# Kernel optimization log

Hardware: AMD Instinct MI355X
Metric: run time of the kernel (lower is better)

## Reference

```python
import jax, jax.numpy as jnp
import numpy as np

DIM = 1024
B, S = 4, 4096

def setup_inputs() -> dict:
    key = jax.random.key(0)
    ks = jax.random.split(key, 8)
    scale = 1.0 / np.sqrt(DIM)
    x = jax.random.normal(ks[0], (B, S, DIM), dtype=jnp.float32)
    Wk = jax.random.normal(ks[1], (DIM, DIM), dtype=jnp.float32) * scale
    Wv = jax.random.normal(ks[2], (DIM, DIM), dtype=jnp.float32) * scale
    Wr = jax.random.normal(ks[3], (DIM, DIM), dtype=jnp.float32) * scale
    Wo = jax.random.normal(ks[4], (DIM, DIM), dtype=jnp.float32) * scale
    time_decay = jax.random.normal(ks[5], (DIM,), dtype=jnp.float32) * 0.01 - 5.0
    time_first = jax.random.normal(ks[6], (DIM,), dtype=jnp.float32) * 0.01
    return {"x": x, "Wk": Wk, "Wv": Wv, "Wr": Wr, "Wo": Wo,
            "time_decay": time_decay, "time_first": time_first}

def reference(x, Wk, Wv, Wr, Wo, time_decay, time_first):
    # Projections (Linear with weight [out, in]: y = x @ W^T)
    k = jnp.einsum('bsd,ed->bse', x, Wk)
    v = jnp.einsum('bsd,ed->bse', x, Wv)
    r = jax.nn.sigmoid(jnp.einsum('bsd,ed->bse', x, Wr))
    w = -jnp.exp(time_decay)          # (D,)
    decay = jnp.exp(w)                # exp(w), per-channel decay in (0,1)
    eu = jnp.exp(time_first)          # exp(u)
    kv = k * v                        # (B, S, D)

    def step(state, kv_t):
        wkv = state + eu * kv_t       # output numerator this step
        new_state = decay * state + kv_t
        return new_state, wkv

    state0 = jnp.zeros((x.shape[0], x.shape[2]), dtype=x.dtype)
    # scan over time axis: move S to leading dim
    _, wkv_seq = jax.lax.scan(step, state0, jnp.swapaxes(kv, 0, 1))  # (S, B, D)
    out = r * jnp.swapaxes(wkv_seq, 0, 1)  # (B, S, D)
    return jnp.einsum('bsd,ed->bse', out, Wo)
```

## Files before the change

### kernel.cpp

```cpp
#include <hip/hip_runtime.h>
#include <hip/hip_bf16.h>

#define DIMD   1024
#define BATCH  4
#define SEQ    4096
#define NTOK   (BATCH * SEQ)
#define CHUNK  64
#define NCHUNK (SEQ / CHUNK)

#define BM 128
#define BN 128
#define BK 32
#define BNF 64

typedef unsigned short ushort_t;
typedef __attribute__((ext_vector_type(8))) __bf16   bf16x8;
typedef __attribute__((ext_vector_type(4))) float    f32x4;
typedef __attribute__((ext_vector_type(8))) ushort_t u16x8;

__device__ __forceinline__ float b2f(ushort_t u) {
    union { unsigned int i; float f; } x;
    x.i = ((unsigned int)u) << 16;
    return x.f;
}

__device__ __forceinline__ ushort_t f2b(float f) {
    union { float f; unsigned int i; } x;
    x.f = f;
    unsigned int r = x.i + 0x7fffu + ((x.i >> 16) & 1u);
    return (ushort_t)(r >> 16);
}

__global__ __launch_bounds__(256)
void conv_f2b(const float* __restrict__ src, ushort_t* __restrict__ dst, int n8)
{
    const int i = blockIdx.x * 256 + threadIdx.x;
    if (i >= n8) return;
    const float4* s4 = (const float4*)src;
    const float4 a = s4[i * 2];
    const float4 b = s4[i * 2 + 1];
    u16x8 o;
    o[0] = f2b(a.x); o[1] = f2b(a.y); o[2] = f2b(a.z); o[3] = f2b(a.w);
    o[4] = f2b(b.x); o[5] = f2b(b.y); o[6] = f2b(b.z); o[7] = f2b(b.w);
    *(u16x8*)(dst + (size_t)i * 8) = o;
}

__global__ __launch_bounds__(256)
void conv_w(const float* __restrict__ W0, const float* __restrict__ W1,
            const float* __restrict__ W2, const float* __restrict__ W3,
            ushort_t* __restrict__ dst)
{
    const int m = blockIdx.y;
    const float* src = (m == 0) ? W0 : (m == 1) ? W1 : (m == 2) ? W2 : W3;
    const int i = blockIdx.x * 256 + threadIdx.x;
    const float4* s4 = (const float4*)src;
    const float4 a = s4[i * 2];
    const float4 b = s4[i * 2 + 1];
    u16x8 o;
    o[0] = f2b(a.x); o[1] = f2b(a.y); o[2] = f2b(a.z); o[3] = f2b(a.w);
    o[4] = f2b(b.x); o[5] = f2b(b.y); o[6] = f2b(b.z); o[7] = f2b(b.w);
    *(u16x8*)(dst + (size_t)m * DIMD * DIMD + (size_t)i * 8) = o;
}

__global__ __launch_bounds__(256, 2)
void gemm_kvr(const ushort_t* __restrict__ A,
              const ushort_t* __restrict__ Wk,
              const ushort_t* __restrict__ Wv,
              const ushort_t* __restrict__ Wr,
              const float* __restrict__ td,
              ushort_t* __restrict__ Okv,
              ushort_t* __restrict__ Or,
              float* __restrict__ cs)
{
    __shared__ __align__(16) ushort_t As[BM * BK];
    __shared__ __align__(16) ushort_t Bk[BNF * BK];
    __shared__ __align__(16) ushort_t Bv[BNF * BK];
    __shared__ __align__(16) ushort_t Br[BNF * BK];

    const int tid  = threadIdx.x;
    const int lane = tid & 63;
    const int wv   = tid >> 6;
    const int wr   = wv >> 1;
    const int wc   = wv & 1;
    const int lrow = lane & 15;
    const int kq   = lane >> 4;

    const int row0 = blockIdx.x * BM;
    const int e0   = blockIdx.y * BNF;

    f32x4 ak[4][2], av[4][2], ar[4][2];
#pragma unroll
    for (int i = 0; i < 4; i++)
#pragma unroll
        for (int j = 0; j < 2; j++) {
            ak[i][j] = f32x4{0.f, 0.f, 0.f, 0.f};
            av[i][j] = f32x4{0.f, 0.f, 0.f, 0.f};
            ar[i][j] = f32x4{0.f, 0.f, 0.f, 0.f};
        }

    for (int kt = 0; kt < DIMD / BK; ++kt) {
        const int k0 = kt * BK;

        __syncthreads();

#pragma unroll
        for (int it = 0; it < 2; ++it) {
            const int chunk = tid + it * 256;
            const int r = chunk >> 2;
            const int c = (chunk & 3) << 3;
            const ushort_t* ga = A + (size_t)(row0 + r) * DIMD + k0 + c;
            __builtin_amdgcn_global_load_lds(
                (__attribute__((address_space(1))) void*)ga,
                (__attribute__((address_space(3))) void*)((char*)As + chunk * 16),
                16, 0, 0);
        }
        {
            const int r = tid >> 2;
            const int c = (tid & 3) << 3;
            const size_t go = (size_t)(e0 + r) * DIMD + k0 + c;
            __builtin_amdgcn_global_load_lds(
                (__attribute__((address_space(1))) void*)(Wk + go),
                (__attribute__((address_space(3))) void*)((char*)Bk + tid * 16),
                16, 0, 0);
            __builtin_amdgcn_global_load_lds(
                (__attribute__((address_space(1))) void*)(Wv + go),
                (__attribute__((address_space(3))) void*)((char*)Bv + tid * 16),
                16, 0, 0);
            __builtin_amdgcn_global_load_lds(
                (__attribute__((address_space(1))) void*)(Wr + go),
                (__attribute__((address_space(3))) void*)((char*)Br + tid * 16),
                16, 0, 0);
        }

        __syncthreads();

        bf16x8 af[4], bk4[2], bv4[2], br4[2];
#pragma unroll
        for (int i = 0; i < 4; i++)
            af[i] = *(const bf16x8*)(As + (wr * 64 + i * 16 + lrow) * BK + kq * 8);
#pragma unroll
        for (int j = 0; j < 2; j++) {
            const int bo = (wc * 32 + j * 16 + lrow) * BK + kq * 8;
            bk4[j] = *(const bf16x8*)(Bk + bo);
            bv4[j] = *(const bf16x8*)(Bv + bo);
            br4[j] = *(const bf16x8*)(Br + bo);
        }

#pragma unroll
        for (int i = 0; i < 4; i++)
#pragma unroll
            for (int j = 0; j < 2; j++) {
                ak[i][j] = __builtin_amdgcn_mfma_f32_16x16x32_bf16(
                    af[i], bk4[j], ak[i][j], 0, 0, 0);
                av[i][j] = __builtin_amdgcn_mfma_f32_16x16x32_bf16(
                    af[i], bv4[j], av[i][j], 0, 0, 0);
                ar[i][j] = __builtin_amdgcn_mfma_f32_16x16x32_bf16(
                    af[i], br4[j], ar[i][j], 0, 0, 0);
            }
    }

#pragma unroll
    for (int i = 0; i < 4; i++)
#pragma unroll
        for (int j = 0; j < 2; j++)
#pragma unroll
            for (int r = 0; r < 4; r++) {
                const int row = row0 + wr * 64 + i * 16 + kq * 4 + r;
                const int col = e0 + wc * 32 + j * 16 + lrow;
                const size_t o = (size_t)row * DIMD + col;
                Okv[o] = f2b(ak[i][j][r] * av[i][j][r]);
                Or[o]  = f2b(1.f / (1.f + __expf(-ar[i][j][r])));
            }

#pragma unroll
    for (int j = 0; j < 2; j++) {
        const int col = e0 + wc * 32 + j * 16 + lrow;
        const float w = -__expf(td[col]);
        float s = 0.f;
#pragma unroll
        for (int i = 0; i < 4; i++)
#pragma unroll
            for (int r = 0; r < 4; r++) {
                const int rl = i * 16 + kq * 4 + r;
                s += __expf(w * (float)(63 - rl)) * ak[i][j][r] * av[i][j][r];
            }
        s += __shfl_xor(s, 16);
        s += __shfl_xor(s, 32);
        if (kq == 0) {
            const int gchunk = (row0 >> 6) + wr;
            cs[(size_t)gchunk * DIMD + col] = s;
        }
    }
}

__global__ __launch_bounds__(256, 2)
void gemm_bt(const ushort_t* __restrict__ A,
             const ushort_t* __restrict__ W,
             float* __restrict__ Of)
{
    __shared__ __align__(16) ushort_t As[BM * BK];
    __shared__ __align__(16) ushort_t Bs[BN * BK];

    const int tid  = threadIdx.x;
    const int lane = tid & 63;
    const int wv   = tid >> 6;
    const int wr   = wv >> 1;
    const int wc   = wv & 1;
    const int lrow = lane & 15;
    const int kq   = lane >> 4;

    const int row0 = blockIdx.x * BM;
    const int e0   = blockIdx.y * BN;

    f32x4 acc[4][4];
#pragma unroll
    for (int i = 0; i < 4; i++)
#pragma unroll
        for (int j = 0; j < 4; j++)
            acc[i][j] = f32x4{0.f, 0.f, 0.f, 0.f};

    for (int kt = 0; kt < DIMD / BK; ++kt) {
        const int k0 = kt * BK;

        __syncthreads();

#pragma unroll
        for (int it = 0; it < 2; ++it) {
            const int chunk = tid + it * 256;
            const int r = chunk >> 2;
            const int c = (chunk & 3) << 3;
            const ushort_t* ga = A + (size_t)(row0 + r) * DIMD + k0 + c;
            const ushort_t* gb = W + (size_t)(e0 + r) * DIMD + k0 + c;
            __builtin_amdgcn_global_load_lds(
                (__attribute__((address_space(1))) void*)ga,
                (__attribute__((address_space(3))) void*)((char*)As + chunk * 16),
                16, 0, 0);
            __builtin_amdgcn_global_load_lds(
                (__attribute__((address_space(1))) void*)gb,
                (__attribute__((address_space(3))) void*)((char*)Bs + chunk * 16),
                16, 0, 0);
        }

        __syncthreads();

        bf16x8 af[4], bfr[4];
#pragma unroll
        for (int i = 0; i < 4; i++)
            af[i] = *(const bf16x8*)(As + (wr * 64 + i * 16 + lrow) * BK + kq * 8);
#pragma unroll
        for (int j = 0; j < 4; j++)
            bfr[j] = *(const bf16x8*)(Bs + (wc * 64 + j * 16 + lrow) * BK + kq * 8);

#pragma unroll
        for (int i = 0; i < 4; i++)
#pragma unroll
            for (int j = 0; j < 4; j++)
                acc[i][j] = __builtin_amdgcn_mfma_f32_16x16x32_bf16(
                    af[i], bfr[j], acc[i][j], 0, 0, 0);
    }

#pragma unroll
    for (int i = 0; i < 4; i++)
#pragma unroll
        for (int j = 0; j < 4; j++)
#pragma unroll
            for (int r = 0; r < 4; r++) {
                const int row = row0 + wr * 64 + i * 16 + kq * 4 + r;
                const int col = e0 + wc * 64 + j * 16 + lrow;
                Of[(size_t)row * DIMD + col] = acc[i][j][r];
            }
}

__global__ __launch_bounds__(256)
void chunk_scan(float* __restrict__ cs, const float* __restrict__ td)
{
    const int idx = blockIdx.x * 256 + threadIdx.x;
    const int d = idx & (DIMD - 1);
    const int b = idx >> 10;

    const float w      = -__expf(td[d]);
    const float decayL = __expf(w * (float)CHUNK);

    float v[NCHUNK];
    const size_t base = ((size_t)b * NCHUNK) * DIMD + d;
#pragma unroll
    for (int c = 0; c < NCHUNK; c++)
        v[c] = cs[base + (size_t)c * DIMD];

    float st = 0.f;
#pragma unroll
    for (int c = 0; c < NCHUNK; c++) {
        const float sc = v[c];
        v[c] = st;
        st = decayL * st + sc;
    }

#pragma unroll
    for (int c = 0; c < NCHUNK; c++)
        cs[base + (size_t)c * DIMD] = v[c];
}

__global__ __launch_bounds__(256)
void emit(const ushort_t* __restrict__ kvb, const ushort_t* __restrict__ rb,
          const float* __restrict__ td, const float* __restrict__ tf,
          const float* __restrict__ cs, ushort_t* __restrict__ op)
{
    const int t  = blockIdx.x * 256 + threadIdx.x;
    const int d0 = (t & (DIMD / 8 - 1)) * 8;
    const int bc = t >> 7;
    const int c  = bc & (NCHUNK - 1);
    const int b  = bc >> 6;

    float decay[8], eu[8], st[8];
#pragma unroll
    for (int j = 0; j < 8; j++) {
        decay[j] = __expf(-__expf(td[d0 + j]));
        eu[j]    = __expf(tf[d0 + j]);
    }
    const float* csp = cs + ((size_t)bc * DIMD + d0);
    const float4 s0 = *(const float4*)csp;
    const float4 s1 = *(const float4*)(csp + 4);
    st[0] = s0.x; st[1] = s0.y; st[2] = s0.z; st[3] = s0.w;
    st[4] = s1.x; st[5] = s1.y; st[6] = s1.z; st[7] = s1.w;

    size_t off = ((size_t)b * SEQ + (size_t)c * CHUNK) * DIMD + d0;
#pragma unroll 8
    for (int i = 0; i < CHUNK; i++) {
        const u16x8 kv8 = *(const u16x8*)(kvb + off);
        const u16x8 r8  = *(const u16x8*)(rb + off);
        u16x8 o8;
#pragma unroll
        for (int j = 0; j < 8; j++) {
            const float kv = b2f(kv8[j]);
            o8[j] = f2b(b2f(r8[j]) * (st[j] + eu[j] * kv));
            st[j] = decay[j] * st[j] + kv;
        }
        *(u16x8*)(op + off) = o8;
        off += DIMD;
    }
}

extern "C" void kernel_launch(void* const* d_in, const int* in_sizes, int n_in,
                              void* d_out, int out_size, void* d_ws, size_t ws_size,
                              hipStream_t stream)
{
    const float* x  = (const float*)d_in[0];
    const float* Wk = (const float*)d_in[1];
    const float* Wv = (const float*)d_in[2];
    const float* Wr = (const float*)d_in[3];
    const float* Wo = (const float*)d_in[4];
    const float* td = (const float*)d_in[5];
    const float* tf = (const float*)d_in[6];

    ushort_t* xb  = (ushort_t*)d_ws;
    ushort_t* Wb  = xb + (size_t)NTOK * DIMD;
    ushort_t* Wkb = Wb;
    ushort_t* Wvb = Wb + (size_t)DIMD * DIMD;
    ushort_t* Wrb = Wb + 2 * (size_t)DIMD * DIMD;
    ushort_t* Wob = Wb + 3 * (size_t)DIMD * DIMD;
    float*    cs  = (float*)(Wb + 4 * (size_t)DIMD * DIMD);
    ushort_t* pbuf = xb;

    ushort_t* kvb = (ushort_t*)d_out;
    ushort_t* rb  = kvb + (size_t)NTOK * DIMD;
    float*    out = (float*)d_out;

    conv_f2b<<<NTOK * DIMD / 8 / 256, 256, 0, stream>>>(x, xb, NTOK * DIMD / 8);
    conv_w<<<dim3(DIMD * DIMD / 8 / 256, 4), 256, 0, stream>>>(Wk, Wv, Wr, Wo, Wb);

    gemm_kvr<<<dim3(NTOK / BM, DIMD / BNF), 256, 0, stream>>>(
        xb, Wkb, Wvb, Wrb, td, kvb, rb, cs);

    chunk_scan<<<BATCH * DIMD / 256, 256, 0, stream>>>(cs, td);

    emit<<<BATCH * NCHUNK * (DIMD / 8) / 256, 256, 0, stream>>>(
        kvb, rb, td, tf, cs, pbuf);

    gemm_bt<<<dim3(NTOK / BM, DIMD / BN), 256, 0, stream>>>(pbuf, Wob, out);
}
```

Before: 319.9 us.

## Merge conversion kernels, enlarge kvr GEMM tile, fold chunk scan into emit

Combines the x and weight bf16 conversion kernels into a single launch. Doubles the gemm_kvr row tile to 256 with 512-thread blocks (8 waves) so each staged weight tile is reused across more rows. Removes the separate chunk_scan kernel: each emit thread recomputes its starting state by sequentially folding the preceding chunk sums. This drops two launches and a read-write pass over cs, at the cost of redundant O(chunk index) work per emit thread and possible occupancy pressure from launch_bounds(512,4).

```diff
diff --git a/kernel.cpp b/kernel.cpp
--- a/kernel.cpp
+++ b/kernel.cpp
@@ -8,10 +8,11 @@
 #define CHUNK  64
 #define NCHUNK (SEQ / CHUNK)
 
+#define BMF 256
+#define BNF 64
 #define BM 128
 #define BN 128
 #define BK 32
-#define BNF 64
 
 typedef unsigned short ushort_t;
 typedef __attribute__((ext_vector_type(8))) __bf16   bf16x8;
@@ -31,38 +32,37 @@
     return (ushort_t)(r >> 16);
 }
 
+#define XU (NTOK * DIMD / 8)
+#define WU (DIMD * DIMD / 8)
 __global__ __launch_bounds__(256)
-void conv_f2b(const float* __restrict__ src, ushort_t* __restrict__ dst, int n8)
+void conv_all(const float* __restrict__ x,
+              const float* __restrict__ W0, const float* __restrict__ W1,
+              const float* __restrict__ W2, const float* __restrict__ W3,
+              ushort_t* __restrict__ xb, ushort_t* __restrict__ Wb)
 {
     const int i = blockIdx.x * 256 + threadIdx.x;
-    if (i >= n8) return;
+    const float* src;
+    ushort_t* dst;
+    int u;
+    if (i < XU) {
+        src = x; dst = xb; u = i;
+    } else {
+        const int wi = i - XU;
+        const int m = wi >> 17;
+        u = wi & (WU - 1);
+        src = (m == 0) ? W0 : (m == 1) ? W1 : (m == 2) ? W2 : W3;
+        dst = Wb + (size_t)m * DIMD * DIMD;
+    }
     const float4* s4 = (const float4*)src;
-    const float4 a = s4[i * 2];
-    const float4 b = s4[i * 2 + 1];
+    const float4 a = s4[(size_t)u * 2];
+    const float4 b = s4[(size_t)u * 2 + 1];
     u16x8 o;
     o[0] = f2b(a.x); o[1] = f2b(a.y); o[2] = f2b(a.z); o[3] = f2b(a.w);
     o[4] = f2b(b.x); o[5] = f2b(b.y); o[6] = f2b(b.z); o[7] = f2b(b.w);
-    *(u16x8*)(dst + (size_t)i * 8) = o;
-}
-
-__global__ __launch_bounds__(256)
-void conv_w(const float* __restrict__ W0, const float* __restrict__ W1,
-            const float* __restrict__ W2, const float* __restrict__ W3,
-            ushort_t* __restrict__ dst)
-{
-    const int m = blockIdx.y;
-    const float* src = (m == 0) ? W0 : (m == 1) ? W1 : (m == 2) ? W2 : W3;
-    const int i = blockIdx.x * 256 + threadIdx.x;
-    const float4* s4 = (const float4*)src;
-    const float4 a = s4[i * 2];
-    const float4 b = s4[i * 2 + 1];
-    u16x8 o;
-    o[0] = f2b(a.x); o[1] = f2b(a.y); o[2] = f2b(a.z); o[3] = f2b(a.w);
-    o[4] = f2b(b.x); o[5] = f2b(b.y); o[6] = f2b(b.z); o[7] = f2b(b.w);
-    *(u16x8*)(dst + (size_t)m * DIMD * DIMD + (size_t)i * 8) = o;
-}
-
-__global__ __launch_bounds__(256, 2)
+    *(u16x8*)(dst + (size_t)u * 8) = o;
+}
+
+__global__ __launch_bounds__(512, 4)
 void gemm_kvr(const ushort_t* __restrict__ A,
               const ushort_t* __restrict__ Wk,
               const ushort_t* __restrict__ Wv,
@@ -72,7 +72,7 @@
               ushort_t* __restrict__ Or,
               float* __restrict__ cs)
 {
-    __shared__ __align__(16) ushort_t As[BM * BK];
+    __shared__ __align__(16) ushort_t As[BMF * BK];
     __shared__ __align__(16) ushort_t Bk[BNF * BK];
     __shared__ __align__(16) ushort_t Bv[BNF * BK];
     __shared__ __align__(16) ushort_t Br[BNF * BK];
@@ -80,12 +80,12 @@
     const int tid  = threadIdx.x;
     const int lane = tid & 63;
     const int wv   = tid >> 6;
-    const int wr   = wv >> 1;
-    const int wc   = wv & 1;
+    const int wr   = wv & 3;
+    const int wc   = wv >> 2;
     const int lrow = lane & 15;
     const int kq   = lane >> 4;
 
-    const int row0 = blockIdx.x * BM;
+    const int row0 = blockIdx.x * BMF;
     const int e0   = blockIdx.y * BNF;
 
     f32x4 ak[4][2], av[4][2], ar[4][2];
@@ -105,7 +105,7 @@
 
 #pragma unroll
         for (int it = 0; it < 2; ++it) {
-            const int chunk = tid + it * 256;
+            const int chunk = tid + it * 512;
             const int r = chunk >> 2;
             const int c = (chunk & 3) << 3;
             const ushort_t* ga = A + (size_t)(row0 + r) * DIMD + k0 + c;
@@ -114,7 +114,7 @@
                 (__attribute__((address_space(3))) void*)((char*)As + chunk * 16),
                 16, 0, 0);
         }
-        {
+        if (tid < 256) {
             const int r = tid >> 2;
             const int c = (tid & 3) << 3;
             const size_t go = (size_t)(e0 + r) * DIMD + k0 + c;
@@ -123,12 +123,17 @@
                 (__attribute__((address_space(3))) void*)((char*)Bk + tid * 16),
                 16, 0, 0);
             __builtin_amdgcn_global_load_lds(
-                (__attribute__((address_space(1))) void*)(Wv + go),
-                (__attribute__((address_space(3))) void*)((char*)Bv + tid * 16),
-                16, 0, 0);
-            __builtin_amdgcn_global_load_lds(
                 (__attribute__((address_space(1))) void*)(Wr + go),
                 (__attribute__((address_space(3))) void*)((char*)Br + tid * 16),
+                16, 0, 0);
+        } else {
+            const int t2 = tid - 256;
+            const int r = t2 >> 2;
+            const int c = (t2 & 3) << 3;
+            const size_t go = (size_t)(e0 + r) * DIMD + k0 + c;
+            __builtin_amdgcn_global_load_lds(
+                (__attribute__((address_space(1))) void*)(Wv + go),
+                (__attribute__((address_space(3))) void*)((char*)Bv + t2 * 16),
                 16, 0, 0);
         }
 
@@ -187,7 +192,7 @@
         s += __shfl_xor(s, 16);
         s += __shfl_xor(s, 32);
         if (kq == 0) {
-            const int gchunk = (row0 >> 6) + wr;
+            const int gchunk = blockIdx.x * 4 + wr;
             cs[(size_t)gchunk * DIMD + col] = s;
         }
     }
@@ -272,35 +277,6 @@
 }
 
 __global__ __launch_bounds__(256)
-void chunk_scan(float* __restrict__ cs, const float* __restrict__ td)
-{
-    const int idx = blockIdx.x * 256 + threadIdx.x;
-    const int d = idx & (DIMD - 1);
-    const int b = idx >> 10;
-
-    const float w      = -__expf(td[d]);
-    const float decayL = __expf(w * (float)CHUNK);
-
-    float v[NCHUNK];
-    const size_t base = ((size_t)b * NCHUNK) * DIMD + d;
-#pragma unroll
-    for (int c = 0; c < NCHUNK; c++)
-        v[c] = cs[base + (size_t)c * DIMD];
-
-    float st = 0.f;
-#pragma unroll
-    for (int c = 0; c < NCHUNK; c++) {
-        const float sc = v[c];
-        v[c] = st;
-        st = decayL * st + sc;
-    }
-
-#pragma unroll
-    for (int c = 0; c < NCHUNK; c++)
-        cs[base + (size_t)c * DIMD] = v[c];
-}
-
-__global__ __launch_bounds__(256)
 void emit(const ushort_t* __restrict__ kvb, const ushort_t* __restrict__ rb,
           const float* __restrict__ td, const float* __restrict__ tf,
           const float* __restrict__ cs, ushort_t* __restrict__ op)
@@ -311,17 +287,25 @@
     const int c  = bc & (NCHUNK - 1);
     const int b  = bc >> 6;
 
-    float decay[8], eu[8], st[8];
+    float w[8], decay[8], decayL[8], eu[8], st[8];
 #pragma unroll
     for (int j = 0; j < 8; j++) {
-        decay[j] = __expf(-__expf(td[d0 + j]));
-        eu[j]    = __expf(tf[d0 + j]);
-    }
-    const float* csp = cs + ((size_t)bc * DIMD + d0);
-    const float4 s0 = *(const float4*)csp;
-    const float4 s1 = *(const float4*)(csp + 4);
-    st[0] = s0.x; st[1] = s0.y; st[2] = s0.z; st[3] = s0.w;
-    st[4] = s1.x; st[5] = s1.y; st[6] = s1.z; st[7] = s1.w;
+        w[j]      = -__expf(td[d0 + j]);
+        decay[j]  = __expf(w[j]);
+        decayL[j] = __expf(w[j] * (float)CHUNK);
+        eu[j]     = __expf(tf[d0 + j]);
+        st[j]     = 0.f;
+    }
+
+    for (int cc = 0; cc < c; ++cc) {
+        const float* sp = cs + (((size_t)b * NCHUNK + cc) * DIMD + d0);
+        const float4 s0 = *(const float4*)sp;
+        const float4 s1 = *(const float4*)(sp + 4);
+        st[0] = decayL[0] * st[0] + s0.x;  st[1] = decayL[1] * st[1] + s0.y;
+        st[2] = decayL[2] * st[2] + s0.z;  st[3] = decayL[3] * st[3] + s0.w;
+        st[4] = decayL[4] * st[4] + s1.x;  st[5] = decayL[5] * st[5] + s1.y;
+        st[6] = decayL[6] * st[6] + s1.z;  st[7] = decayL[7] * st[7] + s1.w;
+    }
 
     size_t off = ((size_t)b * SEQ + (size_t)c * CHUNK) * DIMD + d0;
 #pragma unroll 8
@@ -365,13 +349,10 @@
     ushort_t* rb  = kvb + (size_t)NTOK * DIMD;
     float*    out = (float*)d_out;
 
-    conv_f2b<<<NTOK * DIMD / 8 / 256, 256, 0, stream>>>(x, xb, NTOK * DIMD / 8);
-    conv_w<<<dim3(DIMD * DIMD / 8 / 256, 4), 256, 0, stream>>>(Wk, Wv, Wr, Wo, Wb);
-
-    gemm_kvr<<<dim3(NTOK / BM, DIMD / BNF), 256, 0, stream>>>(
+    conv_all<<<(XU + 4 * WU) / 256, 256, 0, stream>>>(x, Wk, Wv, Wr, Wo, xb, Wb);
+
+    gemm_kvr<<<dim3(NTOK / BMF, DIMD / BNF), 512, 0, stream>>>(
         xb, Wkb, Wvb, Wrb, td, kvb, rb, cs);
-
-    chunk_scan<<<BATCH * DIMD / 256, 256, 0, stream>>>(cs, td);
 
     emit<<<BATCH * NCHUNK * (DIMD / 8) / 256, 256, 0, stream>>>(
         kvb, rb, td, tf, cs, pbuf);
```

Result: slower. 513.2 us (+60.4%).
